# Kernel tuning notes

Hardware: AMD Instinct MI355X
Metric: run time of the kernel (lower is better)

## Reference

```python
import jax, jax.numpy as jnp
import numpy as np

D_MODEL = 1024
NUM_HEADS = 16
OMEGA_0 = 30.0
D_K = D_MODEL // NUM_HEADS


def _siren_uniform(key, shape, fan_in, omega_0=OMEGA_0):
    bound = np.sqrt(6.0 / fan_in) / omega_0
    return jax.random.uniform(key, shape, minval=-bound, maxval=bound, dtype=jnp.float32)


def setup_inputs() -> dict:
    key = jax.random.key(0)
    ks = jax.random.split(key, 9)
    B, S = 2, 2048
    x = jax.random.normal(ks[0], (B, S, D_MODEL), dtype=jnp.float32)
    # weights stored as (out, in) like torch nn.Linear
    Wq = _siren_uniform(ks[1], (D_MODEL, D_MODEL), D_MODEL)
    bq = _siren_uniform(ks[2], (D_MODEL,), D_MODEL)
    Wk = _siren_uniform(ks[3], (D_MODEL, D_MODEL), D_MODEL)
    bk = _siren_uniform(ks[4], (D_MODEL,), D_MODEL)
    Wv = _siren_uniform(ks[5], (D_MODEL, D_MODEL), D_MODEL)
    bv = _siren_uniform(ks[6], (D_MODEL,), D_MODEL)
    Wo = _siren_uniform(ks[7], (D_MODEL, D_MODEL), D_MODEL)
    bo = _siren_uniform(ks[8], (D_MODEL,), D_MODEL)
    return {"x": x, "Wq": Wq, "bq": bq, "Wk": Wk, "bk": bk,
            "Wv": Wv, "bv": bv, "Wo": Wo, "bo": bo}


def reference(x, Wq, bq, Wk, bk, Wv, bv, Wo, bo):
    B, S, _ = x.shape
    scale = np.sqrt(D_K).astype(np.float32)
    # project and split heads: (B, H, S, d_k)
    def proj(W, b):
        y = jnp.einsum('bsd,ed->bse', x, W) + b
        return y.reshape(B, S, NUM_HEADS, D_K).transpose(0, 2, 1, 3)
    Q = proj(Wq, bq)
    K = proj(Wk, bk)
    V = proj(Wv, bv)
    logits = jnp.einsum('bhqd,bhkd->bhqk', Q, K) / scale
    attn = jnp.sin(OMEGA_0 * logits)  # no normalization
    out = jnp.einsum('bhqk,bhkd->bhqd', attn, V)
    out = out.transpose(0, 2, 1, 3).reshape(B, S, D_MODEL)
    return jnp.einsum('bsd,ed->bse', out, Wo) + bo
```

## Files before the change

kernel.cpp:

```cpp
#include <hip/hip_runtime.h>
#include <stdint.h>

typedef __attribute__((ext_vector_type(8))) __bf16 fragAB;
typedef __attribute__((ext_vector_type(4))) float f32x4;

__device__ __forceinline__ unsigned short f2bf(float f) {
    union { float f; unsigned int u; } v; v.f = f;
    unsigned int u = v.u + 0x7fffu + ((v.u >> 16) & 1u);
    return (unsigned short)(u >> 16);
}

__device__ __forceinline__ f32x4 MFMA(fragAB a, fragAB b, f32x4 c) {
    return __builtin_amdgcn_mfma_f32_16x16x32_bf16(a, b, c, 0, 0, 0);
}

__device__ __forceinline__ void gl16(const void* g, void* l) {
    __builtin_amdgcn_global_load_lds((const __attribute__((address_space(1))) void*)g,
                                     (__attribute__((address_space(3))) void*)l, 16, 0, 0);
}

__device__ __forceinline__ float fsin_rev(float rev) {
    float r; asm("v_sin_f32 %0, %1" : "=v"(r) : "v"(rev)); return r;
}
__device__ __forceinline__ unsigned int cvtpk(float lo, float hi) {
    unsigned int r; asm("v_cvt_pk_bf16_f32 %0, %1, %2" : "=v"(r) : "v"(lo), "v"(hi)); return r;
}

__global__ __launch_bounds__(256) void cvt_all(
    const float* __restrict__ x,  const float* __restrict__ wq, const float* __restrict__ wk,
    const float* __restrict__ wv, const float* __restrict__ wo,
    unsigned short* __restrict__ xb,  unsigned short* __restrict__ wqb, unsigned short* __restrict__ wkb,
    unsigned short* __restrict__ wvb, unsigned short* __restrict__ wob)
{
    const int bid = blockIdx.x;
    const float* s; unsigned short* d; int off;
    if (bid < 4096)      { s = x;  d = xb;  off = bid; }
    else if (bid < 5120) { s = wq; d = wqb; off = bid - 4096; }
    else if (bid < 6144) { s = wk; d = wkb; off = bid - 5120; }
    else if (bid < 7168) { s = wv; d = wvb; off = bid - 6144; }
    else                 { s = wo; d = wob; off = bid - 7168; }
    const int i = (off * 256 + threadIdx.x) * 4;
    float4 f = *(const float4*)(s + i);
    ushort4 o;
    o.x = f2bf(f.x); o.y = f2bf(f.y); o.z = f2bf(f.z); o.w = f2bf(f.w);
    *(ushort4*)(d + i) = o;
}

__global__ __launch_bounds__(256, 2)
void gemm_k(const unsigned short* __restrict__ A,
            const unsigned short* __restrict__ W0, const unsigned short* __restrict__ W1,
            const unsigned short* __restrict__ W2,
            const float* __restrict__ b0, const float* __restrict__ b1, const float* __restrict__ b2,
            void* o0, void* o1, void* o2)
{
    __shared__ unsigned short As[8192];
    __shared__ unsigned short Ws[8192];

    const int z = blockIdx.z;
    const unsigned short* W = z == 0 ? W0 : (z == 1 ? W1 : W2);
    const float* bias        = z == 0 ? b0 : (z == 1 ? b1 : b2);
    void* out                = z == 0 ? o0 : (z == 1 ? o1 : o2);
    const int mode           = z == 2 ? 1 : 0;

    const int t = threadIdx.x;
    const int lane = t & 63;
    const int g = lane >> 4;
    const int c = lane & 15;
    const int w = t >> 6;
    const int wm = (w >> 1) * 64;
    const int wn = (w & 1) * 64;
    const int m0 = blockIdx.y * 128;
    const int n0 = blockIdx.x * 128;

    const int srow = lane >> 3;
    const int scol = (lane & 7) * 8;

    const f32x4 zz = {0.f, 0.f, 0.f, 0.f};
    f32x4 acc[4][4];
#pragma unroll
    for (int mi = 0; mi < 4; ++mi)
#pragma unroll
        for (int ni = 0; ni < 4; ++ni) acc[mi][ni] = zz;

    for (int kt = 0; kt < 16; ++kt) {
        const int k0 = kt * 64;
#pragma unroll
        for (int r = 0; r < 4; ++r) {
            gl16(A + (size_t)(m0 + 32 * w + 8 * r + srow) * 1024 + k0 + scol,
                 (unsigned short*)As + (w * 4 + r) * 512);
            gl16(W + (size_t)(n0 + 32 * w + 8 * r + srow) * 1024 + k0 + scol,
                 (unsigned short*)Ws + (w * 4 + r) * 512);
        }
        __syncthreads();
#pragma unroll
        for (int kk = 0; kk < 2; ++kk) {
            fragAB af[4], bfr[4];
#pragma unroll
            for (int mi = 0; mi < 4; ++mi)
                af[mi] = *(const fragAB*)((char*)As + (wm + mi * 16 + c) * 128 + kk * 64 + g * 16);
#pragma unroll
            for (int ni = 0; ni < 4; ++ni)
                bfr[ni] = *(const fragAB*)((char*)Ws + (wn + ni * 16 + c) * 128 + kk * 64 + g * 16);
#pragma unroll
            for (int mi = 0; mi < 4; ++mi)
#pragma unroll
                for (int ni = 0; ni < 4; ++ni)
                    acc[mi][ni] = MFMA(af[mi], bfr[ni], acc[mi][ni]);
        }
        __syncthreads();
    }

    float bv[4];
#pragma unroll
    for (int ni = 0; ni < 4; ++ni) bv[ni] = bias[n0 + wn + ni * 16 + c];

    if (mode == 0) {
        unsigned short* C = (unsigned short*)out;
#pragma unroll
        for (int mi = 0; mi < 4; ++mi)
#pragma unroll
            for (int ni = 0; ni < 4; ++ni)
#pragma unroll
                for (int j = 0; j < 4; ++j) {
                    const int grow = m0 + wm + mi * 16 + g * 4 + j;
                    const int gcol = n0 + wn + ni * 16 + c;
                    C[(size_t)grow * 1024 + gcol] = f2bf(acc[mi][ni][j] + bv[ni]);
                }
    } else {
        unsigned short* Vt = (unsigned short*)out;
#pragma unroll
        for (int mi = 0; mi < 4; ++mi)
#pragma unroll
            for (int ni = 0; ni < 4; ++ni) {
                const int gcol = n0 + wn + ni * 16 + c;
                const int mrow = m0 + wm + mi * 16 + g * 4;
                const int bb = mrow >> 11;
                const int s = mrow & 2047;
                ushort4 pk;
                pk.x = f2bf(acc[mi][ni][0] + bv[ni]);
                pk.y = f2bf(acc[mi][ni][1] + bv[ni]);
                pk.z = f2bf(acc[mi][ni][2] + bv[ni]);
                pk.w = f2bf(acc[mi][ni][3] + bv[ni]);
                *(ushort4*)(Vt + ((size_t)bb * 1024 + gcol) * 2048 + s) = pk;
            }
    }
}

__global__ __launch_bounds__(256, 4)
void gemm64(const unsigned short* __restrict__ A,
            const unsigned short* __restrict__ W,
            const float* __restrict__ bias, float* __restrict__ out)
{
    __shared__ unsigned short As[4096];
    __shared__ unsigned short Ws[8192];

    const int t = threadIdx.x;
    const int lane = t & 63;
    const int g = lane >> 4;
    const int c = lane & 15;
    const int w = t >> 6;
    const int wm = (w >> 1) * 32;
    const int wn = (w & 1) * 64;
    const int m0 = blockIdx.y * 64;
    const int n0 = blockIdx.x * 128;

    const int srow = lane >> 3;
    const int scol = (lane & 7) * 8;

    const f32x4 zz = {0.f, 0.f, 0.f, 0.f};
    f32x4 acc[2][4];
#pragma unroll
    for (int mi = 0; mi < 2; ++mi)
#pragma unroll
        for (int ni = 0; ni < 4; ++ni) acc[mi][ni] = zz;

    for (int kt = 0; kt < 16; ++kt) {
        const int k0 = kt * 64;
        gl16(A + (size_t)(m0 + 16 * w + srow) * 1024 + k0 + scol,
             (unsigned short*)As + (2 * w) * 512);
        gl16(A + (size_t)(m0 + 16 * w + 8 + srow) * 1024 + k0 + scol,
             (unsigned short*)As + (2 * w + 1) * 512);
#pragma unroll
        for (int r = 0; r < 4; ++r)
            gl16(W + (size_t)(n0 + 32 * w + 8 * r + srow) * 1024 + k0 + scol,
                 (unsigned short*)Ws + (w * 4 + r) * 512);
        __syncthreads();
#pragma unroll
        for (int kk = 0; kk < 2; ++kk) {
            fragAB af[2], bfr[4];
#pragma unroll
            for (int mi = 0; mi < 2; ++mi)
                af[mi] = *(const fragAB*)((char*)As + (wm + mi * 16 + c) * 128 + kk * 64 + g * 16);
#pragma unroll
            for (int ni = 0; ni < 4; ++ni)
                bfr[ni] = *(const fragAB*)((char*)Ws + (wn + ni * 16 + c) * 128 + kk * 64 + g * 16);
#pragma unroll
            for (int mi = 0; mi < 2; ++mi)
#pragma unroll
                for (int ni = 0; ni < 4; ++ni)
                    acc[mi][ni] = MFMA(af[mi], bfr[ni], acc[mi][ni]);
        }
        __syncthreads();
    }

#pragma unroll
    for (int ni = 0; ni < 4; ++ni) {
        const float bv = bias[n0 + wn + ni * 16 + c];
#pragma unroll
        for (int mi = 0; mi < 2; ++mi)
#pragma unroll
            for (int j = 0; j < 4; ++j) {
                const int grow = m0 + wm + mi * 16 + g * 4 + j;
                const int gcol = n0 + wn + ni * 16 + c;
                out[(size_t)grow * 1024 + gcol] = acc[mi][ni][j] + bv;
            }
    }
}

#define SWZ(byteoff, row) ((byteoff) ^ (((row) & 7) << 4))
#define SIN_SC 0.5968310366f

__global__ __launch_bounds__(256, 4)
void attn_kernel(const unsigned short* __restrict__ Qg,
                 const unsigned short* __restrict__ Kg,
                 const unsigned short* __restrict__ Vg,
                 unsigned short* __restrict__ AO)
{
    __shared__ unsigned short Ks[2 * 4096];
    __shared__ unsigned short Vs[2 * 4096];
    __shared__ unsigned short Ps[4096];

    const int t = threadIdx.x;
    const int lane = t & 63;
    const int g = lane >> 4;
    const int c = lane & 15;
    const int w = t >> 6;

    const int bid = blockIdx.x;
    const int lb = (bid & 7) * 128 + (bid >> 3);
    const int qb = lb & 31;
    const int h = (lb >> 5) & 15;
    const int b = lb >> 9;
    const int qbase = qb * 64;

    char* const Ksb = (char*)Ks;
    char* const Vsb = (char*)Vs;
    char* const Psb = (char*)Ps;

    const int r8 = lane >> 3;
    const int col8 = (lane & 7) ^ r8;
    const unsigned short* KgB = Kg + (size_t)(b * 2048) * 1024 + h * 64;
    const unsigned short* VtB = Vg + ((size_t)b * 1024 + h * 64) * 2048;
    const int ch0 = 2 * w, ch1 = 2 * w + 1;

    fragAB qreg[2][4];
#pragma unroll
    for (int kk = 0; kk < 2; ++kk)
#pragma unroll
        for (int qi = 0; qi < 4; ++qi)
            qreg[kk][qi] = *(const fragAB*)(Qg + (size_t)(b * 2048 + qbase + qi * 16 + c) * 1024
                                            + h * 64 + kk * 32 + g * 8);

    gl16(KgB + (size_t)(8 * ch0 + r8) * 1024 + col8 * 8, (unsigned short*)Ks + ch0 * 512);
    gl16(KgB + (size_t)(8 * ch1 + r8) * 1024 + col8 * 8, (unsigned short*)Ks + ch1 * 512);
    gl16(VtB + (size_t)(8 * ch0 + r8) * 2048 + col8 * 8, (unsigned short*)Vs + ch0 * 512);
    gl16(VtB + (size_t)(8 * ch1 + r8) * 2048 + col8 * 8, (unsigned short*)Vs + ch1 * 512);
    __syncthreads();

    const f32x4 z = {0.f, 0.f, 0.f, 0.f};
    f32x4 o[4];
#pragma unroll
    for (int ni = 0; ni < 4; ++ni) o[ni] = z;

    const int krow = 16 * w + c;
    const int pkbyte = (16 * w + g * 4) * 2;

    for (int kb = 0; kb < 32; ++kb) {
        const int cur = kb & 1;
        char* const kc = Ksb + cur * 8192;
        char* const vc = Vsb + cur * 8192;

        if (kb < 31) {
            const int nxt = cur ^ 1;
            unsigned short* kl = (unsigned short*)Ks + nxt * 4096;
            unsigned short* vl = (unsigned short*)Vs + nxt * 4096;
            const size_t kro = (size_t)(kb + 1) * 64;
            gl16(KgB + (kro + 8 * ch0 + r8) * 1024 + col8 * 8, kl + ch0 * 512);
            gl16(KgB + (kro + 8 * ch1 + r8) * 1024 + col8 * 8, kl + ch1 * 512);
            gl16(VtB + (size_t)(8 * ch0 + r8) * 2048 + kro + col8 * 8, vl + ch0 * 512);
            gl16(VtB + (size_t)(8 * ch1 + r8) * 2048 + kro + col8 * 8, vl + ch1 * 512);
        }

        fragAB kf0 = *(const fragAB*)(kc + SWZ(krow * 128 + g * 16, krow));
        fragAB kf1 = *(const fragAB*)(kc + SWZ(krow * 128 + 64 + g * 16, krow));
        f32x4 st[4];
#pragma unroll
        for (int qi = 0; qi < 4; ++qi) st[qi] = z;
#pragma unroll
        for (int qi = 0; qi < 4; ++qi) {
            st[qi] = MFMA(kf0, qreg[0][qi], st[qi]);
            st[qi] = MFMA(kf1, qreg[1][qi], st[qi]);
        }

#pragma unroll
        for (int qi = 0; qi < 4; ++qi) {
            const int q = qi * 16 + c;
            float s0 = fsin_rev(st[qi][0] * SIN_SC);
            float s1 = fsin_rev(st[qi][1] * SIN_SC);
            float s2 = fsin_rev(st[qi][2] * SIN_SC);
            float s3 = fsin_rev(st[qi][3] * SIN_SC);
            uint2 pk;
            pk.x = cvtpk(s0, s1);
            pk.y = cvtpk(s2, s3);
            *(uint2*)(Psb + SWZ(q * 128 + pkbyte, q)) = pk;
        }

        asm volatile("s_waitcnt lgkmcnt(0)" ::: "memory");
        __builtin_amdgcn_s_barrier();

#pragma unroll
        for (int kk = 0; kk < 2; ++kk) {
            fragAB pf, vf[4];
            pf = *(const fragAB*)(Psb + SWZ(krow * 128 + kk * 64 + g * 16, krow));
#pragma unroll
            for (int ni = 0; ni < 4; ++ni) {
                const int dd = ni * 16 + c;
                vf[ni] = *(const fragAB*)(vc + SWZ(dd * 128 + kk * 64 + g * 16, dd));
            }
#pragma unroll
            for (int ni = 0; ni < 4; ++ni)
                o[ni] = MFMA(pf, vf[ni], o[ni]);
        }

        __syncthreads();
    }

#pragma unroll
    for (int ni = 0; ni < 4; ++ni) {
        const int dd = ni * 16 + c;
#pragma unroll
        for (int j = 0; j < 4; ++j) {
            const int q = qbase + 16 * w + g * 4 + j;
            AO[(size_t)(b * 2048 + q) * 1024 + h * 64 + dd] = f2bf(o[ni][j]);
        }
    }
}

extern "C" void kernel_launch(void* const* d_in, const int* in_sizes, int n_in,
                              void* d_out, int out_size, void* d_ws, size_t ws_size,
                              hipStream_t stream) {
    (void)in_sizes; (void)n_in; (void)out_size; (void)ws_size;
    const float* x  = (const float*)d_in[0];
    const float* Wq = (const float*)d_in[1];
    const float* bq = (const float*)d_in[2];
    const float* Wk = (const float*)d_in[3];
    const float* bk = (const float*)d_in[4];
    const float* Wv = (const float*)d_in[5];
    const float* bv = (const float*)d_in[6];
    const float* Wo = (const float*)d_in[7];
    const float* bo = (const float*)d_in[8];

    char* ws = (char*)d_ws;
    unsigned short* xb  = (unsigned short*)(ws);
    unsigned short* Wqb = (unsigned short*)(ws + (8u  << 20));
    unsigned short* Wkb = (unsigned short*)(ws + (10u << 20));
    unsigned short* Wvb = (unsigned short*)(ws + (12u << 20));
    unsigned short* Wob = (unsigned short*)(ws + (14u << 20));
    unsigned short* Qb  = (unsigned short*)(ws + (16u << 20));
    unsigned short* Kb  = (unsigned short*)(ws + (24u << 20));
    unsigned short* Vtb = (unsigned short*)(ws + (32u << 20));
    unsigned short* AO  = (unsigned short*)(ws + (40u << 20));

    cvt_all<<<8192, 256, 0, stream>>>(x, Wq, Wk, Wv, Wo, xb, Wqb, Wkb, Wvb, Wob);

    gemm_k<<<dim3(8, 32, 3), 256, 0, stream>>>(xb, Wqb, Wkb, Wvb, bq, bk, bv,
                                               Qb, Kb, Vtb);

    attn_kernel<<<1024, 256, 0, stream>>>(Qb, Kb, Vtb, AO);

    gemm64<<<dim3(8, 64), 256, 0, stream>>>(AO, Wob, bo, (float*)d_out);
}
```

Baseline: 116.3 us.

## Load K/V fragments directly from global into registers with 128-query tiles

The attention kernel drops the shared-memory K and V staging buffers. Each wave now loads its K and V MFMA fragments straight from global memory into registers, with K prefetched one block ahead through a ping-pong register pair. The query tile per block grows from 64 to 128, which halves the grid and doubles the reuse of each K/V block, and launch bounds drop to 2 blocks per SIMD. Only the P staging buffer stays in LDS, so there are fewer barriers and LDS round trips, but global traffic becomes uncoalesced and register pressure goes up.

```diff
diff --git a/kernel.cpp b/kernel.cpp
--- a/kernel.cpp
+++ b/kernel.cpp
@@ -220,15 +220,13 @@
 #define SWZ(byteoff, row) ((byteoff) ^ (((row) & 7) << 4))
 #define SIN_SC 0.5968310366f
 
-__global__ __launch_bounds__(256, 4)
+__global__ __launch_bounds__(256, 2)
 void attn_kernel(const unsigned short* __restrict__ Qg,
                  const unsigned short* __restrict__ Kg,
                  const unsigned short* __restrict__ Vg,
                  unsigned short* __restrict__ AO)
 {
-    __shared__ unsigned short Ks[2 * 4096];
-    __shared__ unsigned short Vs[2 * 4096];
-    __shared__ unsigned short Ps[4096];
+    __shared__ unsigned short Ps[8192];
 
     const int t = threadIdx.x;
     const int lane = t & 63;
@@ -237,73 +235,61 @@
     const int w = t >> 6;
 
     const int bid = blockIdx.x;
-    const int lb = (bid & 7) * 128 + (bid >> 3);
-    const int qb = lb & 31;
-    const int h = (lb >> 5) & 15;
-    const int b = lb >> 9;
-    const int qbase = qb * 64;
-
-    char* const Ksb = (char*)Ks;
-    char* const Vsb = (char*)Vs;
+    const int lb = (bid & 7) * 64 + (bid >> 3);
+    const int qb = lb & 15;
+    const int h = (lb >> 4) & 15;
+    const int b = lb >> 8;
+    const int qbase = qb * 128;
+
     char* const Psb = (char*)Ps;
 
-    const int r8 = lane >> 3;
-    const int col8 = (lane & 7) ^ r8;
-    const unsigned short* KgB = Kg + (size_t)(b * 2048) * 1024 + h * 64;
-    const unsigned short* VtB = Vg + ((size_t)b * 1024 + h * 64) * 2048;
-    const int ch0 = 2 * w, ch1 = 2 * w + 1;
-
-    fragAB qreg[2][4];
+    fragAB qreg[2][8];
 #pragma unroll
     for (int kk = 0; kk < 2; ++kk)
 #pragma unroll
-        for (int qi = 0; qi < 4; ++qi)
+        for (int qi = 0; qi < 8; ++qi)
             qreg[kk][qi] = *(const fragAB*)(Qg + (size_t)(b * 2048 + qbase + qi * 16 + c) * 1024
                                             + h * 64 + kk * 32 + g * 8);
 
-    gl16(KgB + (size_t)(8 * ch0 + r8) * 1024 + col8 * 8, (unsigned short*)Ks + ch0 * 512);
-    gl16(KgB + (size_t)(8 * ch1 + r8) * 1024 + col8 * 8, (unsigned short*)Ks + ch1 * 512);
-    gl16(VtB + (size_t)(8 * ch0 + r8) * 2048 + col8 * 8, (unsigned short*)Vs + ch0 * 512);
-    gl16(VtB + (size_t)(8 * ch1 + r8) * 2048 + col8 * 8, (unsigned short*)Vs + ch1 * 512);
-    __syncthreads();
+    const unsigned short* Kbase = Kg + (size_t)(b * 2048 + 16 * w + c) * 1024 + h * 64 + g * 8;
+    const unsigned short* Vbase = Vg + ((size_t)b * 1024 + h * 64 + c) * 2048 + g * 8;
 
     const f32x4 z = {0.f, 0.f, 0.f, 0.f};
-    f32x4 o[4];
-#pragma unroll
-    for (int ni = 0; ni < 4; ++ni) o[ni] = z;
-
-    const int krow = 16 * w + c;
-    const int pkbyte = (16 * w + g * 4) * 2;
-
-    for (int kb = 0; kb < 32; ++kb) {
-        const int cur = kb & 1;
-        char* const kc = Ksb + cur * 8192;
-        char* const vc = Vsb + cur * 8192;
-
+    f32x4 o[2][4];
+#pragma unroll
+    for (int mi = 0; mi < 2; ++mi)
+#pragma unroll
+        for (int ni = 0; ni < 4; ++ni) o[mi][ni] = z;
+
+    const int pkbyte = 32 * w + 8 * g;
+
+    fragAB kfA[2], kfB[2];
+    kfA[0] = *(const fragAB*)(Kbase);
+    kfA[1] = *(const fragAB*)(Kbase + 32);
+
+    auto body = [&](int kb, fragAB (&kfc)[2], fragAB (&kfn)[2]) {
         if (kb < 31) {
-            const int nxt = cur ^ 1;
-            unsigned short* kl = (unsigned short*)Ks + nxt * 4096;
-            unsigned short* vl = (unsigned short*)Vs + nxt * 4096;
-            const size_t kro = (size_t)(kb + 1) * 64;
-            gl16(KgB + (kro + 8 * ch0 + r8) * 1024 + col8 * 8, kl + ch0 * 512);
-            gl16(KgB + (kro + 8 * ch1 + r8) * 1024 + col8 * 8, kl + ch1 * 512);
-            gl16(VtB + (size_t)(8 * ch0 + r8) * 2048 + kro + col8 * 8, vl + ch0 * 512);
-            gl16(VtB + (size_t)(8 * ch1 + r8) * 2048 + kro + col8 * 8, vl + ch1 * 512);
-        }
-
-        fragAB kf0 = *(const fragAB*)(kc + SWZ(krow * 128 + g * 16, krow));
-        fragAB kf1 = *(const fragAB*)(kc + SWZ(krow * 128 + 64 + g * 16, krow));
-        f32x4 st[4];
-#pragma unroll
-        for (int qi = 0; qi < 4; ++qi) st[qi] = z;
-#pragma unroll
-        for (int qi = 0; qi < 4; ++qi) {
-            st[qi] = MFMA(kf0, qreg[0][qi], st[qi]);
-            st[qi] = MFMA(kf1, qreg[1][qi], st[qi]);
-        }
-
-#pragma unroll
-        for (int qi = 0; qi < 4; ++qi) {
+            kfn[0] = *(const fragAB*)(Kbase + (size_t)(kb + 1) * 65536);
+            kfn[1] = *(const fragAB*)(Kbase + (size_t)(kb + 1) * 65536 + 32);
+        }
+        fragAB vf[2][4];
+#pragma unroll
+        for (int kk = 0; kk < 2; ++kk)
+#pragma unroll
+            for (int ni = 0; ni < 4; ++ni)
+                vf[kk][ni] = *(const fragAB*)(Vbase + (size_t)(ni * 16) * 2048 + kb * 64 + kk * 32);
+
+        f32x4 st[8];
+#pragma unroll
+        for (int qi = 0; qi < 8; ++qi) st[qi] = z;
+#pragma unroll
+        for (int qi = 0; qi < 8; ++qi) {
+            st[qi] = MFMA(kfc[0], qreg[0][qi], st[qi]);
+            st[qi] = MFMA(kfc[1], qreg[1][qi], st[qi]);
+        }
+
+#pragma unroll
+        for (int qi = 0; qi < 8; ++qi) {
             const int q = qi * 16 + c;
             float s0 = fsin_rev(st[qi][0] * SIN_SC);
             float s1 = fsin_rev(st[qi][1] * SIN_SC);
@@ -320,30 +306,38 @@
 
 #pragma unroll
         for (int kk = 0; kk < 2; ++kk) {
-            fragAB pf, vf[4];
-            pf = *(const fragAB*)(Psb + SWZ(krow * 128 + kk * 64 + g * 16, krow));
-#pragma unroll
-            for (int ni = 0; ni < 4; ++ni) {
-                const int dd = ni * 16 + c;
-                vf[ni] = *(const fragAB*)(vc + SWZ(dd * 128 + kk * 64 + g * 16, dd));
+            fragAB pf[2];
+#pragma unroll
+            for (int mi = 0; mi < 2; ++mi) {
+                const int q = 32 * w + mi * 16 + c;
+                pf[mi] = *(const fragAB*)(Psb + SWZ(q * 128 + kk * 64 + g * 16, q));
             }
 #pragma unroll
-            for (int ni = 0; ni < 4; ++ni)
-                o[ni] = MFMA(pf, vf[ni], o[ni]);
-        }
-
-        __syncthreads();
-    }
-
-#pragma unroll
-    for (int ni = 0; ni < 4; ++ni) {
-        const int dd = ni * 16 + c;
-#pragma unroll
-        for (int j = 0; j < 4; ++j) {
-            const int q = qbase + 16 * w + g * 4 + j;
-            AO[(size_t)(b * 2048 + q) * 1024 + h * 64 + dd] = f2bf(o[ni][j]);
-        }
-    }
+            for (int mi = 0; mi < 2; ++mi)
+#pragma unroll
+                for (int ni = 0; ni < 4; ++ni)
+                    o[mi][ni] = MFMA(pf[mi], vf[kk][ni], o[mi][ni]);
+        }
+
+        __builtin_amdgcn_s_barrier();
+    };
+
+    for (int tt = 0; tt < 16; ++tt) {
+        body(2 * tt,     kfA, kfB);
+        body(2 * tt + 1, kfB, kfA);
+    }
+
+#pragma unroll
+    for (int mi = 0; mi < 2; ++mi)
+#pragma unroll
+        for (int ni = 0; ni < 4; ++ni) {
+            const int dd = ni * 16 + c;
+#pragma unroll
+            for (int j = 0; j < 4; ++j) {
+                const int q = qbase + 32 * w + mi * 16 + g * 4 + j;
+                AO[(size_t)(b * 2048 + q) * 1024 + h * 64 + dd] = f2bf(o[mi][ni][j]);
+            }
+        }
 }
 
 extern "C" void kernel_launch(void* const* d_in, const int* in_sizes, int n_in,
@@ -376,7 +370,7 @@
     gemm_k<<<dim3(8, 32, 3), 256, 0, stream>>>(xb, Wqb, Wkb, Wvb, bq, bk, bv,
                                                Qb, Kb, Vtb);
 
-    attn_kernel<<<1024, 256, 0, stream>>>(Qb, Kb, Vtb, AO);
+    attn_kernel<<<512, 256, 0, stream>>>(Qb, Kb, Vtb, AO);
 
     gemm64<<<dim3(8, 64), 256, 0, stream>>>(AO, Wob, bo, (float*)d_out);
 }
```

Measured after the change: 145.4 us. +25.0%, slower.
